# Optimization experiments

Hardware: AMD Instinct MI355X
Metric: run time of the kernel (lower is better)

Reference implementation:

```python
import jax, jax.numpy as jnp
import numpy as np

N, E = 50000, 800000
D_IN, D_HID, D_OUT = 128, 256, 128


def setup_inputs() -> dict:
    key = jax.random.key(0)
    k = jax.random.split(key, 7)
    x = jax.random.normal(k[0], (N, D_IN), dtype=jnp.float32)
    edge_src = jax.random.randint(k[1], (E,), 0, N, dtype=jnp.int32)
    edge_dst = jax.random.randint(k[2], (E,), 0, N, dtype=jnp.int32)
    s1 = 1.0 / np.sqrt(2 * D_IN)
    s2 = 1.0 / np.sqrt(2 * D_HID)
    W1 = jax.random.uniform(k[3], (2 * D_IN, D_HID), jnp.float32, -s1, s1)
    b1 = jax.random.uniform(k[4], (D_HID,), jnp.float32, -s1, s1)
    W2 = jax.random.uniform(k[5], (2 * D_HID, D_OUT), jnp.float32, -s2, s2)
    b2 = jax.random.uniform(k[6], (D_OUT,), jnp.float32, -s2, s2)
    return {"x": x, "edge_src": edge_src, "edge_dst": edge_dst,
            "W1": W1, "b1": b1, "W2": W2, "b2": b2}


def _sage_layer(h, edge_src, edge_dst, W, b, inv_deg):
    # mean-pool neighbor features: gather [E, D] then segment-sum to [N, D]
    msgs = h[edge_src]
    agg = jax.ops.segment_sum(msgs, edge_dst, num_segments=h.shape[0]) * inv_deg
    y = jnp.concatenate([h, agg], axis=1)  # [N, 2D]
    return y @ W + b


def reference(x, edge_src, edge_dst, W1, b1, W2, b2):
    n = x.shape[0]
    deg = jax.ops.segment_sum(jnp.ones_like(edge_dst, dtype=x.dtype), edge_dst,
                              num_segments=n)
    inv_deg = (1.0 / jnp.maximum(deg, 1.0))[:, None]  # isolated nodes -> zeros
    h = _sage_layer(x, edge_src, edge_dst, W1, b1, inv_deg)
    h = jax.nn.relu(h)
    # dropout is identity in eval mode
    h = _sage_layer(h, edge_src, edge_dst, W2, b2, inv_deg)
    return jax.nn.log_softmax(h, axis=1)
```

## Files before the change

kernel.cpp:

```cpp
#include <hip/hip_runtime.h>
#include <cstdint>
#include <cstddef>

typedef __attribute__((ext_vector_type(8))) short bf16x8;
typedef __attribute__((ext_vector_type(4))) float f32x4;
typedef __attribute__((ext_vector_type(2))) float f32x2;

__device__ inline short bf16_rne(float f) {
  unsigned u = __builtin_bit_cast(unsigned, f);
  u += 0x7fff + ((u >> 16) & 1);
  return (short)(u >> 16);
}

__device__ inline float bf16lo(unsigned v) { return __builtin_bit_cast(float, v << 16); }
__device__ inline float bf16hi(unsigned v) { return __builtin_bit_cast(float, v & 0xffff0000u); }

__device__ inline unsigned pack2(float a, float b) {
  return ((unsigned)(unsigned short)bf16_rne(a)) | (((unsigned)(unsigned short)bf16_rne(b)) << 16);
}

__device__ inline void async_copy16(const void* g, void* l) {
  __builtin_amdgcn_global_load_lds((const __attribute__((address_space(1))) void*)g,
                                   (__attribute__((address_space(3))) void*)l, 16, 0, 0);
}


__global__ __launch_bounds__(256) void bucket_hist(const int* __restrict__ dst, int E, int EPB,
                                                   int* __restrict__ histT, int SB, int NB) {
  __shared__ int h[256];
  int tid = threadIdx.x;
  h[tid] = 0;
  __syncthreads();
  int start = blockIdx.x * EPB, end = min(E, start + EPB);
  for (int i = start + tid; i < end; i += 256) atomicAdd(&h[((unsigned)dst[i]) >> 8], 1);
  __syncthreads();
  if (tid < NB) histT[tid * SB + blockIdx.x] = h[tid];
}

__global__ __launch_bounds__(1024) void scan1_kernel(const int* __restrict__ in,
                                                     int* __restrict__ outx,
                                                     int* __restrict__ part, int n) {
  __shared__ int buf[1024];
  int tid = threadIdx.x;
  int i = blockIdx.x * 1024 + tid;
  int v = (i < n) ? in[i] : 0;
  buf[tid] = v;
  __syncthreads();
  #pragma unroll
  for (int off = 1; off < 1024; off <<= 1) {
    int t = (tid >= off) ? buf[tid - off] : 0;
    __syncthreads();
    buf[tid] += t;
    __syncthreads();
  }
  if (i < n) outx[i] = buf[tid] - v;
  if (tid == 1023) part[blockIdx.x] = buf[1023];
}

__global__ __launch_bounds__(1024) void scan2_kernel(int* __restrict__ part, int B) {
  __shared__ int buf[1024];
  int tid = threadIdx.x;
  int v = (tid < B) ? part[tid] : 0;
  buf[tid] = v;
  __syncthreads();
  #pragma unroll
  for (int off = 1; off < 1024; off <<= 1) {
    int t = (tid >= off) ? buf[tid - off] : 0;
    __syncthreads();
    buf[tid] += t;
    __syncthreads();
  }
  if (tid < B) part[tid] = buf[tid] - v;
}

__global__ __launch_bounds__(256) void bucket_scatter(const int* __restrict__ src,
                                                      const int* __restrict__ dst, int E, int EPB,
                                                      const int* __restrict__ excl,
                                                      const int* __restrict__ part, int SB, int NB,
                                                      unsigned* __restrict__ bedge) {
  __shared__ int cur[256];
  int tid = threadIdx.x;
  for (int t = tid; t < NB; t += 256) cur[t] = excl[t * SB + blockIdx.x] + part[t];
  __syncthreads();
  int start = blockIdx.x * EPB, end = min(E, start + EPB);
  for (int i = start + tid; i < end; i += 256) {
    unsigned d = (unsigned)dst[i];
    int p = atomicAdd(&cur[d >> 8], 1);
    bedge[p] = ((d & 255u) << 24) | (unsigned)src[i];
  }
}

__global__ __launch_bounds__(256) void build_csr(const unsigned* __restrict__ bedge,
                                                 const int* __restrict__ excl,
                                                 const int* __restrict__ part, int SB, int NB,
                                                 int N, int E,
                                                 int* __restrict__ offsets,
                                                 float* __restrict__ inv_deg,
                                                 int* __restrict__ ssrc) {
  __shared__ int buf[256];
  int b = blockIdx.x, tid = threadIdx.x;
  int estart = excl[b * SB] + part[b];
  int eend = (b == NB - 1) ? E : (excl[(b + 1) * SB] + part[b + 1]);
  buf[tid] = 0;
  __syncthreads();
  for (int i = estart + tid; i < eend; i += 256) atomicAdd(&buf[bedge[i] >> 24], 1);
  __syncthreads();
  int cnt = buf[tid];
  #pragma unroll
  for (int off = 1; off < 256; off <<= 1) {
    int t = (tid >= off) ? buf[tid - off] : 0;
    __syncthreads();
    buf[tid] += t;
    __syncthreads();
  }
  int excl_l = buf[tid] - cnt;
  int node = (b << 8) + tid;
  if (node < N) {
    offsets[node] = estart + excl_l;
    inv_deg[node] = 1.0f / fmaxf((float)cnt, 1.0f);
  }
  if (node == N) offsets[N] = E;
  __syncthreads();
  buf[tid] = estart + excl_l;
  __syncthreads();
  for (int i = estart + tid; i < eend; i += 256) {
    unsigned e2 = bedge[i];
    int p = atomicAdd(&buf[e2 >> 24], 1);
    ssrc[p] = (int)(e2 & 0xFFFFFFu);
  }
}

__global__ __launch_bounds__(256) void prep_kernel(const float* __restrict__ W1,
                                                   const float* __restrict__ W2,
                                                   const float* __restrict__ b2,
                                                   const float* __restrict__ x,
                                                   short* __restrict__ B1p,
                                                   short* __restrict__ B2p,
                                                   float* __restrict__ bias2,
                                                   unsigned* __restrict__ A1u, int npairs) {
  int b = blockIdx.x;
  if (b < 512) {
    int mode = b >> 8;
    int idx = (b & 255) * 256 + threadIdx.x;
    int j = idx & 7;
    int L = (idx >> 3) & 63;
    int nt = (idx >> 9) & 15;
    int kb = idx >> 13;
    int k = kb * 32 + (L >> 4) * 8 + j;
    int n = nt * 16 + (L & 15);
    if (mode == 0) {
      B1p[idx] = bf16_rne(W1[(size_t)k * 256 + n]);
    } else {
      float v = (n < 128) ? W2[(size_t)k * 128 + n] : W2[(size_t)(256 + k) * 128 + (n - 128)];
      B2p[idx] = bf16_rne(v);
    }
  } else if (b == 512) {
    int j = threadIdx.x;
    bias2[j] = (j < 128) ? b2[j] : 0.0f;
  } else {
    int idx = (b - 513) * 256 + threadIdx.x;
    if (idx < npairs) {
      int n = idx >> 6, dp = idx & 63;
      float2 v = ((const float2*)x)[idx];
      A1u[(size_t)n * 128 + dp] = pack2(v.x, v.y);
    }
  }
}

__global__ __launch_bounds__(256) void agg1_kernel(const uint2* __restrict__ A2,
                                                   const int* __restrict__ offsets,
                                                   const int* __restrict__ ssrc,
                                                   const float* __restrict__ inv_deg,
                                                   uint2* __restrict__ A2out, int N) {
  int node = blockIdx.x * 4 + (threadIdx.x >> 6);
  if (node >= N) return;
  int lane = threadIdx.x & 63;
  int half = lane >> 5;
  int l = lane & 31;
  int s = offsets[node], e = offsets[node + 1];
  float a0 = 0.f, a1 = 0.f, a2 = 0.f, a3 = 0.f;
  int i = s;
  for (; i + 8 <= e; i += 8) {
    int sA = ssrc[i + half], sB = ssrc[i + 2 + half];
    int sC = ssrc[i + 4 + half], sD = ssrc[i + 6 + half];
    uint2 u = A2[((unsigned)sA << 6) + l];
    uint2 v = A2[((unsigned)sB << 6) + l];
    uint2 w = A2[((unsigned)sC << 6) + l];
    uint2 z = A2[((unsigned)sD << 6) + l];
    a0 += bf16lo(u.x); a1 += bf16hi(u.x); a2 += bf16lo(u.y); a3 += bf16hi(u.y);
    a0 += bf16lo(v.x); a1 += bf16hi(v.x); a2 += bf16lo(v.y); a3 += bf16hi(v.y);
    a0 += bf16lo(w.x); a1 += bf16hi(w.x); a2 += bf16lo(w.y); a3 += bf16hi(w.y);
    a0 += bf16lo(z.x); a1 += bf16hi(z.x); a2 += bf16lo(z.y); a3 += bf16hi(z.y);
  }
  for (; i + 2 <= e; i += 2) {
    int sA = ssrc[i + half];
    uint2 u = A2[((unsigned)sA << 6) + l];
    a0 += bf16lo(u.x); a1 += bf16hi(u.x); a2 += bf16lo(u.y); a3 += bf16hi(u.y);
  }
  if (i < e && half == 0) {
    uint2 u = A2[((unsigned)ssrc[i] << 6) + l];
    a0 += bf16lo(u.x); a1 += bf16hi(u.x); a2 += bf16lo(u.y); a3 += bf16hi(u.y);
  }
  a0 += __shfl_xor(a0, 32, 64);
  a1 += __shfl_xor(a1, 32, 64);
  a2 += __shfl_xor(a2, 32, 64);
  a3 += __shfl_xor(a3, 32, 64);
  if (half == 0) {
    float id = inv_deg[node];
    A2out[((unsigned)node << 6) + 32 + l] =
        make_uint2(pack2(a0 * id, a1 * id), pack2(a2 * id, a3 * id));
  }
}

__global__ __launch_bounds__(256) void gemm_mfma(const short* __restrict__ A,
                                                 const short* __restrict__ Bp,
                                                 const float* __restrict__ bias,
                                                 void* __restrict__ out0,
                                                 void* __restrict__ out1,
                                                 int M_pad, int mode) {
  __shared__ __align__(16) short As[4096];
  __shared__ __align__(16) short Bs[4096];
  int tid = threadIdx.x;
  int w = tid >> 6;
  int lane = tid & 63;
  int wr = w >> 1;
  int wc = w & 1;
  int bm = blockIdx.x * 128;
  int bn = blockIdx.y * 128;

  f32x4 acc[4][4];
  #pragma unroll
  for (int i = 0; i < 4; ++i)
    #pragma unroll
    for (int j = 0; j < 4; ++j) acc[i][j] = (f32x4)(0.0f);

  for (int kb = 0; kb < 8; ++kb) {
    #pragma unroll
    for (int q = 0; q < 2; ++q) {
      int f = q * 4 + w;
      int row = bm + f * 16 + (lane & 15);
      const short* g = A + (size_t)row * 256 + kb * 32 + (lane >> 4) * 8;
      async_copy16(g, &As[f * 512]);
    }
    #pragma unroll
    for (int q = 0; q < 2; ++q) {
      int f = q * 4 + w;
      const short* g = Bp + ((size_t)(kb * 16 + (bn >> 4) + f) * 64 + lane) * 8;
      async_copy16(g, &Bs[f * 512]);
    }
    __syncthreads();

    bf16x8 af[4], bfr[4];
    #pragma unroll
    for (int i = 0; i < 4; ++i)
      af[i] = *(const bf16x8*)&As[(wr * 4 + i) * 512 + lane * 8];
    #pragma unroll
    for (int j = 0; j < 4; ++j)
      bfr[j] = *(const bf16x8*)&Bs[(wc * 4 + j) * 512 + lane * 8];

    #pragma unroll
    for (int i = 0; i < 4; ++i)
      #pragma unroll
      for (int j = 0; j < 4; ++j)
        acc[i][j] = __builtin_amdgcn_mfma_f32_16x16x32_bf16(af[i], bfr[j], acc[i][j], 0, 0, 0);
    __syncthreads();
  }

  int crow0 = (lane >> 4) * 4;
  int ccol = lane & 15;
  #pragma unroll
  for (int i = 0; i < 4; ++i) {
    #pragma unroll
    for (int j = 0; j < 4; ++j) {
      int col_loc = wc * 64 + j * 16 + ccol;
      int col = bn + col_loc;
      #pragma unroll
      for (int r = 0; r < 4; ++r) {
        int row = bm + wr * 64 + i * 16 + crow0 + r;
        float v = acc[i][j][r] + bias[col];
        if (mode == 0) {
          v = fmaxf(v, 0.0f);
          ((short*)out0)[(size_t)row * 256 + col] = bf16_rne(v);
        } else if (blockIdx.y == 0) {
          ((short*)out0)[(size_t)row * 128 + col_loc] = bf16_rne(v);
        } else {
          int pk = __builtin_amdgcn_cvt_pk_fp8_f32(v, v, 0, false);
          ((unsigned char*)out1)[(size_t)row * 128 + col_loc] = (unsigned char)(pk & 0xff);
        }
      }
    }
  }
}

__global__ __launch_bounds__(256) void final_kernel(const uint2* __restrict__ utopU,
                                                    const unsigned* __restrict__ T2,
                                                    const int* __restrict__ offsets,
                                                    const int* __restrict__ ssrc,
                                                    const float* __restrict__ inv_deg,
                                                    float4* __restrict__ out4, int N) {
  int node = blockIdx.x * 4 + (threadIdx.x >> 6);
  if (node >= N) return;
  int lane = threadIdx.x & 63;
  int half = lane >> 5;
  int l = lane & 31;
  int s = offsets[node], e = offsets[node + 1];
  float a0 = 0.f, a1 = 0.f, a2 = 0.f, a3 = 0.f;
  int i = s;
  for (; i + 8 <= e; i += 8) {
    int sA = ssrc[i + half], sB = ssrc[i + 2 + half];
    int sC = ssrc[i + 4 + half], sD = ssrc[i + 6 + half];
    unsigned u = T2[((unsigned)sA << 5) + l];
    unsigned v = T2[((unsigned)sB << 5) + l];
    unsigned w = T2[((unsigned)sC << 5) + l];
    unsigned z = T2[((unsigned)sD << 5) + l];
    f32x2 p, q;
    p = __builtin_amdgcn_cvt_pk_f32_fp8(u, false); q = __builtin_amdgcn_cvt_pk_f32_fp8(u, true);
    a0 += p[0]; a1 += p[1]; a2 += q[0]; a3 += q[1];
    p = __builtin_amdgcn_cvt_pk_f32_fp8(v, false); q = __builtin_amdgcn_cvt_pk_f32_fp8(v, true);
    a0 += p[0]; a1 += p[1]; a2 += q[0]; a3 += q[1];
    p = __builtin_amdgcn_cvt_pk_f32_fp8(w, false); q = __builtin_amdgcn_cvt_pk_f32_fp8(w, true);
    a0 += p[0]; a1 += p[1]; a2 += q[0]; a3 += q[1];
    p = __builtin_amdgcn_cvt_pk_f32_fp8(z, false); q = __builtin_amdgcn_cvt_pk_f32_fp8(z, true);
    a0 += p[0]; a1 += p[1]; a2 += q[0]; a3 += q[1];
  }
  for (; i + 2 <= e; i += 2) {
    unsigned u = T2[((unsigned)ssrc[i + half] << 5) + l];
    f32x2 p = __builtin_amdgcn_cvt_pk_f32_fp8(u, false);
    f32x2 q = __builtin_amdgcn_cvt_pk_f32_fp8(u, true);
    a0 += p[0]; a1 += p[1]; a2 += q[0]; a3 += q[1];
  }
  if (i < e && half == 0) {
    unsigned u = T2[((unsigned)ssrc[i] << 5) + l];
    f32x2 p = __builtin_amdgcn_cvt_pk_f32_fp8(u, false);
    f32x2 q = __builtin_amdgcn_cvt_pk_f32_fp8(u, true);
    a0 += p[0]; a1 += p[1]; a2 += q[0]; a3 += q[1];
  }
  a0 += __shfl_xor(a0, 32, 64);
  a1 += __shfl_xor(a1, 32, 64);
  a2 += __shfl_xor(a2, 32, 64);
  a3 += __shfl_xor(a3, 32, 64);
  if (half == 0) {
    float id = inv_deg[node];
    uint2 u = utopU[((unsigned)node << 5) + l];
    float v0 = bf16lo(u.x) + a0 * id;
    float v1 = bf16hi(u.x) + a1 * id;
    float v2 = bf16lo(u.y) + a2 * id;
    float v3 = bf16hi(u.y) + a3 * id;
    float m = fmaxf(fmaxf(v0, v1), fmaxf(v2, v3));
    #pragma unroll
    for (int off = 1; off < 32; off <<= 1) m = fmaxf(m, __shfl_xor(m, off, 32));
    float su = expf(v0 - m) + expf(v1 - m) + expf(v2 - m) + expf(v3 - m);
    #pragma unroll
    for (int off = 1; off < 32; off <<= 1) su += __shfl_xor(su, off, 32);
    float ls = m + logf(su);
    out4[((unsigned)node << 5) + l] = make_float4(v0 - ls, v1 - ls, v2 - ls, v3 - ls);
  }
}

extern "C" void kernel_launch(void* const* d_in, const int* in_sizes, int n_in,
                              void* d_out, int out_size, void* d_ws, size_t ws_size,
                              hipStream_t stream) {
  const float* x        = (const float*)d_in[0];
  const int*   edge_src = (const int*)d_in[1];
  const int*   edge_dst = (const int*)d_in[2];
  const float* W1       = (const float*)d_in[3];
  const float* b1       = (const float*)d_in[4];
  const float* W2       = (const float*)d_in[5];
  const float* b2       = (const float*)d_in[6];
  float* out = (float*)d_out;

  const int D_IN = 128;
  const int N = in_sizes[0] / D_IN;
  const int E = in_sizes[1];
  const int M_pad = ((N + 127) / 128) * 128;

  const int SB = 1024;
  const int EPB = (E + SB - 1) / SB;
  const int NB = (N + 255) >> 8;
  const int M = NB * SB;
  const int sbl = (M + 1023) / 1024;

  char* ws = (char*)d_ws;
  size_t p = 0;
  auto take = [&](size_t bytes) -> size_t {
    size_t r = p;
    p += (bytes + 255) & ~(size_t)255;
    return r;
  };
  size_t histT_off = take((size_t)M * 4);
  size_t excl_off  = take((size_t)(M + 1) * 4);
  size_t part_off  = take((size_t)1024 * 4);
  size_t bedge_off = take((size_t)E * 4);
  size_t offs_off  = take((size_t)(N + 1) * 4);
  size_t inv_off   = take((size_t)N * 4);
  size_t ssrc_off  = take((size_t)E * 4);
  size_t A1_off    = take((size_t)M_pad * 256 * 2);
  size_t h_off     = take((size_t)M_pad * 256 * 2);
  size_t B1p_off   = take((size_t)256 * 256 * 2);
  size_t B2p_off   = take((size_t)256 * 256 * 2);
  size_t bias2_off = take((size_t)256 * 4);
  size_t utop_off  = take((size_t)M_pad * 128 * 2);
  size_t t2_off    = take((size_t)M_pad * 128);
  (void)ws_size;

  int*   histT   = (int*)(ws + histT_off);
  int*   excl    = (int*)(ws + excl_off);
  int*   part    = (int*)(ws + part_off);
  unsigned* bedge = (unsigned*)(ws + bedge_off);
  int*   offsets = (int*)(ws + offs_off);
  float* inv_deg = (float*)(ws + inv_off);
  int*   ssrc    = (int*)(ws + ssrc_off);
  unsigned* A1u  = (unsigned*)(ws + A1_off);
  short* h       = (short*)(ws + h_off);
  short* B1p     = (short*)(ws + B1p_off);
  short* B2p     = (short*)(ws + B2p_off);
  float* bias2   = (float*)(ws + bias2_off);
  short* utop    = (short*)(ws + utop_off);
  unsigned char* t2f8 = (unsigned char*)(ws + t2_off);

  bucket_hist<<<SB, 256, 0, stream>>>(edge_dst, E, EPB, histT, SB, NB);
  scan1_kernel<<<sbl, 1024, 0, stream>>>(histT, excl, part, M);
  scan2_kernel<<<1, 1024, 0, stream>>>(part, sbl);
  bucket_scatter<<<SB, 256, 0, stream>>>(edge_src, edge_dst, E, EPB, excl, part, SB, NB, bedge);
  build_csr<<<NB, 256, 0, stream>>>(bedge, excl, part, SB, NB, N, E, offsets, inv_deg, ssrc);

  {
    int npairs = N * 64;
    int grid = 513 + (npairs + 255) / 256;
    prep_kernel<<<grid, 256, 0, stream>>>(W1, W2, b2, x, B1p, B2p, bias2, A1u, npairs);
  }

  agg1_kernel<<<(N + 3) / 4, 256, 0, stream>>>((const uint2*)A1u, offsets, ssrc, inv_deg,
                                               (uint2*)A1u, N);
  {
    dim3 grid(M_pad / 128, 2);
    gemm_mfma<<<grid, 256, 0, stream>>>((const short*)A1u, B1p, b1, h, nullptr, M_pad, 0);
  }
  {
    dim3 grid(M_pad / 128, 2);
    gemm_mfma<<<grid, 256, 0, stream>>>(h, B2p, bias2, utop, t2f8, M_pad, 1);
  }
  final_kernel<<<(N + 3) / 4, 256, 0, stream>>>((const uint2*)utop, (const unsigned*)t2f8,
                                                offsets, ssrc, inv_deg, (float4*)out, N);
}
```

Baseline: 240.2 us.

## Gather layer-1 neighbors from FP8 copy of x and widen per-lane gather width

The prep kernel now also writes an FP8 (e4m3) copy of the input features, and the first aggregation gathers neighbor rows from it instead of the bf16 copy, halving gather bytes per edge. Both gather kernels change to four edge-groups of 16 lanes, each loading 8 bytes and accumulating 8 channels, with a two-step shuffle reduction. The CSR bucket size drops from 256 to 128 nodes, giving more build_csr blocks. FP8 quantization of the raw inputs adds error to the layer-1 mean aggregation.

```diff
diff --git a/kernel.cpp b/kernel.cpp
--- a/kernel.cpp
+++ b/kernel.cpp
@@ -27,14 +27,14 @@
 
 __global__ __launch_bounds__(256) void bucket_hist(const int* __restrict__ dst, int E, int EPB,
                                                    int* __restrict__ histT, int SB, int NB) {
-  __shared__ int h[256];
+  __shared__ int h[512];
   int tid = threadIdx.x;
-  h[tid] = 0;
+  for (int t = tid; t < NB; t += 256) h[t] = 0;
   __syncthreads();
   int start = blockIdx.x * EPB, end = min(E, start + EPB);
-  for (int i = start + tid; i < end; i += 256) atomicAdd(&h[((unsigned)dst[i]) >> 8], 1);
-  __syncthreads();
-  if (tid < NB) histT[tid * SB + blockIdx.x] = h[tid];
+  for (int i = start + tid; i < end; i += 256) atomicAdd(&h[((unsigned)dst[i]) >> 7], 1);
+  __syncthreads();
+  for (int t = tid; t < NB; t += 256) histT[t * SB + blockIdx.x] = h[t];
 }
 
 __global__ __launch_bounds__(1024) void scan1_kernel(const int* __restrict__ in,
@@ -78,15 +78,15 @@
                                                       const int* __restrict__ excl,
                                                       const int* __restrict__ part, int SB, int NB,
                                                       unsigned* __restrict__ bedge) {
-  __shared__ int cur[256];
+  __shared__ int cur[512];
   int tid = threadIdx.x;
   for (int t = tid; t < NB; t += 256) cur[t] = excl[t * SB + blockIdx.x] + part[t];
   __syncthreads();
   int start = blockIdx.x * EPB, end = min(E, start + EPB);
   for (int i = start + tid; i < end; i += 256) {
     unsigned d = (unsigned)dst[i];
-    int p = atomicAdd(&cur[d >> 8], 1);
-    bedge[p] = ((d & 255u) << 24) | (unsigned)src[i];
+    int p = atomicAdd(&cur[d >> 7], 1);
+    bedge[p] = ((d & 127u) << 24) | (unsigned)src[i];
   }
 }
 
@@ -97,31 +97,32 @@
                                                  int* __restrict__ offsets,
                                                  float* __restrict__ inv_deg,
                                                  int* __restrict__ ssrc) {
-  __shared__ int buf[256];
+  __shared__ int buf[128];
   int b = blockIdx.x, tid = threadIdx.x;
   int estart = excl[b * SB] + part[b];
   int eend = (b == NB - 1) ? E : (excl[(b + 1) * SB] + part[b + 1]);
-  buf[tid] = 0;
+  if (tid < 128) buf[tid] = 0;
   __syncthreads();
   for (int i = estart + tid; i < eend; i += 256) atomicAdd(&buf[bedge[i] >> 24], 1);
   __syncthreads();
-  int cnt = buf[tid];
+  int cnt = (tid < 128) ? buf[tid] : 0;
   #pragma unroll
-  for (int off = 1; off < 256; off <<= 1) {
-    int t = (tid >= off) ? buf[tid - off] : 0;
-    __syncthreads();
-    buf[tid] += t;
-    __syncthreads();
-  }
-  int excl_l = buf[tid] - cnt;
-  int node = (b << 8) + tid;
-  if (node < N) {
-    offsets[node] = estart + excl_l;
-    inv_deg[node] = 1.0f / fmaxf((float)cnt, 1.0f);
-  }
-  if (node == N) offsets[N] = E;
-  __syncthreads();
-  buf[tid] = estart + excl_l;
+  for (int off = 1; off < 128; off <<= 1) {
+    int t = (tid >= off && tid < 128) ? buf[tid - off] : 0;
+    __syncthreads();
+    if (tid < 128) buf[tid] += t;
+    __syncthreads();
+  }
+  if (tid < 128) {
+    int excl_l = buf[tid] - cnt;
+    int node = (b << 7) + tid;
+    if (node < N) {
+      offsets[node] = estart + excl_l;
+      inv_deg[node] = 1.0f / fmaxf((float)cnt, 1.0f);
+    }
+    if (node == N) offsets[N] = E;
+    buf[tid] = estart + excl_l;
+  }
   __syncthreads();
   for (int i = estart + tid; i < eend; i += 256) {
     unsigned e2 = bedge[i];
@@ -137,7 +138,8 @@
                                                    short* __restrict__ B1p,
                                                    short* __restrict__ B2p,
                                                    float* __restrict__ bias2,
-                                                   unsigned* __restrict__ A1u, int npairs) {
+                                                   unsigned* __restrict__ A1u,
+                                                   unsigned* __restrict__ xf8, int nquads) {
   int b = blockIdx.x;
   if (b < 512) {
     int mode = b >> 8;
@@ -159,56 +161,68 @@
     bias2[j] = (j < 128) ? b2[j] : 0.0f;
   } else {
     int idx = (b - 513) * 256 + threadIdx.x;
-    if (idx < npairs) {
-      int n = idx >> 6, dp = idx & 63;
-      float2 v = ((const float2*)x)[idx];
-      A1u[(size_t)n * 128 + dp] = pack2(v.x, v.y);
-    }
-  }
-}
-
-__global__ __launch_bounds__(256) void agg1_kernel(const uint2* __restrict__ A2,
+    if (idx < nquads) {
+      int n = idx >> 5, q = idx & 31;
+      float4 v = ((const float4*)x)[idx];
+      ((uint2*)A1u)[(size_t)n * 64 + q] = make_uint2(pack2(v.x, v.y), pack2(v.z, v.w));
+      int pk = __builtin_amdgcn_cvt_pk_fp8_f32(v.x, v.y, 0, false);
+      pk = __builtin_amdgcn_cvt_pk_fp8_f32(v.z, v.w, pk, true);
+      xf8[(size_t)n * 32 + q] = (unsigned)pk;
+    }
+  }
+}
+
+
+__global__ __launch_bounds__(256) void agg1_kernel(const uint2* __restrict__ X8,
                                                    const int* __restrict__ offsets,
                                                    const int* __restrict__ ssrc,
                                                    const float* __restrict__ inv_deg,
-                                                   uint2* __restrict__ A2out, int N) {
+                                                   uint4* __restrict__ A1q, int N) {
   int node = blockIdx.x * 4 + (threadIdx.x >> 6);
   if (node >= N) return;
   int lane = threadIdx.x & 63;
-  int half = lane >> 5;
-  int l = lane & 31;
+  int g = lane >> 4;
+  int l = lane & 15;
   int s = offsets[node], e = offsets[node + 1];
-  float a0 = 0.f, a1 = 0.f, a2 = 0.f, a3 = 0.f;
+  float a0=0.f,a1=0.f,a2=0.f,a3=0.f,a4=0.f,a5=0.f,a6=0.f,a7=0.f;
   int i = s;
   for (; i + 8 <= e; i += 8) {
-    int sA = ssrc[i + half], sB = ssrc[i + 2 + half];
-    int sC = ssrc[i + 4 + half], sD = ssrc[i + 6 + half];
-    uint2 u = A2[((unsigned)sA << 6) + l];
-    uint2 v = A2[((unsigned)sB << 6) + l];
-    uint2 w = A2[((unsigned)sC << 6) + l];
-    uint2 z = A2[((unsigned)sD << 6) + l];
-    a0 += bf16lo(u.x); a1 += bf16hi(u.x); a2 += bf16lo(u.y); a3 += bf16hi(u.y);
-    a0 += bf16lo(v.x); a1 += bf16hi(v.x); a2 += bf16lo(v.y); a3 += bf16hi(v.y);
-    a0 += bf16lo(w.x); a1 += bf16hi(w.x); a2 += bf16lo(w.y); a3 += bf16hi(w.y);
-    a0 += bf16lo(z.x); a1 += bf16hi(z.x); a2 += bf16lo(z.y); a3 += bf16hi(z.y);
-  }
-  for (; i + 2 <= e; i += 2) {
-    int sA = ssrc[i + half];
-    uint2 u = A2[((unsigned)sA << 6) + l];
-    a0 += bf16lo(u.x); a1 += bf16hi(u.x); a2 += bf16lo(u.y); a3 += bf16hi(u.y);
-  }
-  if (i < e && half == 0) {
-    uint2 u = A2[((unsigned)ssrc[i] << 6) + l];
-    a0 += bf16lo(u.x); a1 += bf16hi(u.x); a2 += bf16lo(u.y); a3 += bf16hi(u.y);
-  }
-  a0 += __shfl_xor(a0, 32, 64);
-  a1 += __shfl_xor(a1, 32, 64);
-  a2 += __shfl_xor(a2, 32, 64);
-  a3 += __shfl_xor(a3, 32, 64);
-  if (half == 0) {
+    int sA = ssrc[i + g], sB = ssrc[i + 4 + g];
+    uint2 u = X8[((size_t)(unsigned)sA << 4) + l];
+    uint2 v = X8[((size_t)(unsigned)sB << 4) + l];
+    f32x2 p, q;
+    p = __builtin_amdgcn_cvt_pk_f32_fp8(u.x, false); q = __builtin_amdgcn_cvt_pk_f32_fp8(u.x, true);
+    a0 += p[0]; a1 += p[1]; a2 += q[0]; a3 += q[1];
+    p = __builtin_amdgcn_cvt_pk_f32_fp8(u.y, false); q = __builtin_amdgcn_cvt_pk_f32_fp8(u.y, true);
+    a4 += p[0]; a5 += p[1]; a6 += q[0]; a7 += q[1];
+    p = __builtin_amdgcn_cvt_pk_f32_fp8(v.x, false); q = __builtin_amdgcn_cvt_pk_f32_fp8(v.x, true);
+    a0 += p[0]; a1 += p[1]; a2 += q[0]; a3 += q[1];
+    p = __builtin_amdgcn_cvt_pk_f32_fp8(v.y, false); q = __builtin_amdgcn_cvt_pk_f32_fp8(v.y, true);
+    a4 += p[0]; a5 += p[1]; a6 += q[0]; a7 += q[1];
+  }
+  for (; i < e; i += 4) {
+    if (g < e - i) {
+      uint2 u = X8[((size_t)(unsigned)ssrc[i + g] << 4) + l];
+      f32x2 p, q;
+      p = __builtin_amdgcn_cvt_pk_f32_fp8(u.x, false); q = __builtin_amdgcn_cvt_pk_f32_fp8(u.x, true);
+      a0 += p[0]; a1 += p[1]; a2 += q[0]; a3 += q[1];
+      p = __builtin_amdgcn_cvt_pk_f32_fp8(u.y, false); q = __builtin_amdgcn_cvt_pk_f32_fp8(u.y, true);
+      a4 += p[0]; a5 += p[1]; a6 += q[0]; a7 += q[1];
+    }
+  }
+  a0 += __shfl_xor(a0,16,64); a0 += __shfl_xor(a0,32,64);
+  a1 += __shfl_xor(a1,16,64); a1 += __shfl_xor(a1,32,64);
+  a2 += __shfl_xor(a2,16,64); a2 += __shfl_xor(a2,32,64);
+  a3 += __shfl_xor(a3,16,64); a3 += __shfl_xor(a3,32,64);
+  a4 += __shfl_xor(a4,16,64); a4 += __shfl_xor(a4,32,64);
+  a5 += __shfl_xor(a5,16,64); a5 += __shfl_xor(a5,32,64);
+  a6 += __shfl_xor(a6,16,64); a6 += __shfl_xor(a6,32,64);
+  a7 += __shfl_xor(a7,16,64); a7 += __shfl_xor(a7,32,64);
+  if (g == 0) {
     float id = inv_deg[node];
-    A2out[((unsigned)node << 6) + 32 + l] =
-        make_uint2(pack2(a0 * id, a1 * id), pack2(a2 * id, a3 * id));
+    A1q[((size_t)node << 5) + 16 + l] =
+        make_uint4(pack2(a0 * id, a1 * id), pack2(a2 * id, a3 * id),
+                   pack2(a4 * id, a5 * id), pack2(a6 * id, a7 * id));
   }
 }
 
@@ -292,8 +306,8 @@
   }
 }
 
-__global__ __launch_bounds__(256) void final_kernel(const uint2* __restrict__ utopU,
-                                                    const unsigned* __restrict__ T2,
+__global__ __launch_bounds__(256) void final_kernel(const uint4* __restrict__ utopq,
+                                                    const uint2* __restrict__ T2,
                                                     const int* __restrict__ offsets,
                                                     const int* __restrict__ ssrc,
                                                     const float* __restrict__ inv_deg,
@@ -301,59 +315,64 @@
   int node = blockIdx.x * 4 + (threadIdx.x >> 6);
   if (node >= N) return;
   int lane = threadIdx.x & 63;
-  int half = lane >> 5;
-  int l = lane & 31;
+  int g = lane >> 4;
+  int l = lane & 15;
   int s = offsets[node], e = offsets[node + 1];
-  float a0 = 0.f, a1 = 0.f, a2 = 0.f, a3 = 0.f;
+  float a0=0.f,a1=0.f,a2=0.f,a3=0.f,a4=0.f,a5=0.f,a6=0.f,a7=0.f;
   int i = s;
   for (; i + 8 <= e; i += 8) {
-    int sA = ssrc[i + half], sB = ssrc[i + 2 + half];
-    int sC = ssrc[i + 4 + half], sD = ssrc[i + 6 + half];
-    unsigned u = T2[((unsigned)sA << 5) + l];
-    unsigned v = T2[((unsigned)sB << 5) + l];
-    unsigned w = T2[((unsigned)sC << 5) + l];
-    unsigned z = T2[((unsigned)sD << 5) + l];
+    int sA = ssrc[i + g], sB = ssrc[i + 4 + g];
+    uint2 u = T2[((size_t)(unsigned)sA << 4) + l];
+    uint2 v = T2[((size_t)(unsigned)sB << 4) + l];
     f32x2 p, q;
-    p = __builtin_amdgcn_cvt_pk_f32_fp8(u, false); q = __builtin_amdgcn_cvt_pk_f32_fp8(u, true);
+    p = __builtin_amdgcn_cvt_pk_f32_fp8(u.x, false); q = __builtin_amdgcn_cvt_pk_f32_fp8(u.x, true);
     a0 += p[0]; a1 += p[1]; a2 += q[0]; a3 += q[1];
-    p = __builtin_amdgcn_cvt_pk_f32_fp8(v, false); q = __builtin_amdgcn_cvt_pk_f32_fp8(v, true);
+    p = __builtin_amdgcn_cvt_pk_f32_fp8(u.y, false); q = __builtin_amdgcn_cvt_pk_f32_fp8(u.y, true);
+    a4 += p[0]; a5 += p[1]; a6 += q[0]; a7 += q[1];
+    p = __builtin_amdgcn_cvt_pk_f32_fp8(v.x, false); q = __builtin_amdgcn_cvt_pk_f32_fp8(v.x, true);
     a0 += p[0]; a1 += p[1]; a2 += q[0]; a3 += q[1];
-    p = __builtin_amdgcn_cvt_pk_f32_fp8(w, false); q = __builtin_amdgcn_cvt_pk_f32_fp8(w, true);
-    a0 += p[0]; a1 += p[1]; a2 += q[0]; a3 += q[1];
-    p = __builtin_amdgcn_cvt_pk_f32_fp8(z, false); q = __builtin_amdgcn_cvt_pk_f32_fp8(z, true);
-    a0 += p[0]; a1 += p[1]; a2 += q[0]; a3 += q[1];
-  }
-  for (; i + 2 <= e; i += 2) {
-    unsigned u = T2[((unsigned)ssrc[i + half] << 5) + l];
-    f32x2 p = __builtin_amdgcn_cvt_pk_f32_fp8(u, false);
-    f32x2 q = __builtin_amdgcn_cvt_pk_f32_fp8(u, true);
-    a0 += p[0]; a1 += p[1]; a2 += q[0]; a3 += q[1];
-  }
-  if (i < e && half == 0) {
-    unsigned u = T2[((unsigned)ssrc[i] << 5) + l];
-    f32x2 p = __builtin_amdgcn_cvt_pk_f32_fp8(u, false);
-    f32x2 q = __builtin_amdgcn_cvt_pk_f32_fp8(u, true);
-    a0 += p[0]; a1 += p[1]; a2 += q[0]; a3 += q[1];
-  }
-  a0 += __shfl_xor(a0, 32, 64);
-  a1 += __shfl_xor(a1, 32, 64);
-  a2 += __shfl_xor(a2, 32, 64);
-  a3 += __shfl_xor(a3, 32, 64);
-  if (half == 0) {
+    p = __builtin_amdgcn_cvt_pk_f32_fp8(v.y, false); q = __builtin_amdgcn_cvt_pk_f32_fp8(v.y, true);
+    a4 += p[0]; a5 += p[1]; a6 += q[0]; a7 += q[1];
+  }
+  for (; i < e; i += 4) {
+    if (g < e - i) {
+      uint2 u = T2[((size_t)(unsigned)ssrc[i + g] << 4) + l];
+      f32x2 p, q;
+      p = __builtin_amdgcn_cvt_pk_f32_fp8(u.x, false); q = __builtin_amdgcn_cvt_pk_f32_fp8(u.x, true);
+      a0 += p[0]; a1 += p[1]; a2 += q[0]; a3 += q[1];
+      p = __builtin_amdgcn_cvt_pk_f32_fp8(u.y, false); q = __builtin_amdgcn_cvt_pk_f32_fp8(u.y, true);
+      a4 += p[0]; a5 += p[1]; a6 += q[0]; a7 += q[1];
+    }
+  }
+  a0 += __shfl_xor(a0,16,64); a0 += __shfl_xor(a0,32,64);
+  a1 += __shfl_xor(a1,16,64); a1 += __shfl_xor(a1,32,64);
+  a2 += __shfl_xor(a2,16,64); a2 += __shfl_xor(a2,32,64);
+  a3 += __shfl_xor(a3,16,64); a3 += __shfl_xor(a3,32,64);
+  a4 += __shfl_xor(a4,16,64); a4 += __shfl_xor(a4,32,64);
+  a5 += __shfl_xor(a5,16,64); a5 += __shfl_xor(a5,32,64);
+  a6 += __shfl_xor(a6,16,64); a6 += __shfl_xor(a6,32,64);
+  a7 += __shfl_xor(a7,16,64); a7 += __shfl_xor(a7,32,64);
+  if (g == 0) {
     float id = inv_deg[node];
-    uint2 u = utopU[((unsigned)node << 5) + l];
-    float v0 = bf16lo(u.x) + a0 * id;
-    float v1 = bf16hi(u.x) + a1 * id;
-    float v2 = bf16lo(u.y) + a2 * id;
-    float v3 = bf16hi(u.y) + a3 * id;
-    float m = fmaxf(fmaxf(v0, v1), fmaxf(v2, v3));
-    #pragma unroll
-    for (int off = 1; off < 32; off <<= 1) m = fmaxf(m, __shfl_xor(m, off, 32));
-    float su = expf(v0 - m) + expf(v1 - m) + expf(v2 - m) + expf(v3 - m);
-    #pragma unroll
-    for (int off = 1; off < 32; off <<= 1) su += __shfl_xor(su, off, 32);
+    uint4 U = utopq[((size_t)node << 4) + l];
+    float v0 = bf16lo(U.x) + a0 * id;
+    float v1 = bf16hi(U.x) + a1 * id;
+    float v2 = bf16lo(U.y) + a2 * id;
+    float v3 = bf16hi(U.y) + a3 * id;
+    float v4 = bf16lo(U.z) + a4 * id;
+    float v5 = bf16hi(U.z) + a5 * id;
+    float v6 = bf16lo(U.w) + a6 * id;
+    float v7 = bf16hi(U.w) + a7 * id;
+    float m = fmaxf(fmaxf(fmaxf(v0, v1), fmaxf(v2, v3)), fmaxf(fmaxf(v4, v5), fmaxf(v6, v7)));
+    #pragma unroll
+    for (int off = 1; off < 16; off <<= 1) m = fmaxf(m, __shfl_xor(m, off, 16));
+    float su = expf(v0 - m) + expf(v1 - m) + expf(v2 - m) + expf(v3 - m) +
+               expf(v4 - m) + expf(v5 - m) + expf(v6 - m) + expf(v7 - m);
+    #pragma unroll
+    for (int off = 1; off < 16; off <<= 1) su += __shfl_xor(su, off, 16);
     float ls = m + logf(su);
-    out4[((unsigned)node << 5) + l] = make_float4(v0 - ls, v1 - ls, v2 - ls, v3 - ls);
+    out4[((size_t)node << 5) + l * 2]     = make_float4(v0 - ls, v1 - ls, v2 - ls, v3 - ls);
+    out4[((size_t)node << 5) + l * 2 + 1] = make_float4(v4 - ls, v5 - ls, v6 - ls, v7 - ls);
   }
 }
 
@@ -376,7 +395,7 @@
 
   const int SB = 1024;
   const int EPB = (E + SB - 1) / SB;
-  const int NB = (N + 255) >> 8;
+  const int NB = (N + 127) >> 7;
   const int M = NB * SB;
   const int sbl = (M + 1023) / 1024;
 
@@ -395,6 +414,7 @@
   size_t inv_off   = take((size_t)N * 4);
   size_t ssrc_off  = take((size_t)E * 4);
   size_t A1_off    = take((size_t)M_pad * 256 * 2);
+  size_t xf8_off   = take((size_t)M_pad * 128);
   size_t h_off     = take((size_t)M_pad * 256 * 2);
   size_t B1p_off   = take((size_t)256 * 256 * 2);
   size_t B2p_off   = take((size_t)256 * 256 * 2);
@@ -411,6 +431,7 @@
   float* inv_deg = (float*)(ws + inv_off);
   int*   ssrc    = (int*)(ws + ssrc_off);
   unsigned* A1u  = (unsigned*)(ws + A1_off);
+  unsigned* xf8  = (unsigned*)(ws + xf8_off);
   short* h       = (short*)(ws + h_off);
   short* B1p     = (short*)(ws + B1p_off);
   short* B2p     = (short*)(ws + B2p_off);
@@ -425,13 +446,13 @@
   build_csr<<<NB, 256, 0, stream>>>(bedge, excl, part, SB, NB, N, E, offsets, inv_deg, ssrc);
 
   {
-    int npairs = N * 64;
-    int grid = 513 + (npairs + 255) / 256;
-    prep_kernel<<<grid, 256, 0, stream>>>(W1, W2, b2, x, B1p, B2p, bias2, A1u, npairs);
-  }
-
-  agg1_kernel<<<(N + 3) / 4, 256, 0, stream>>>((const uint2*)A1u, offsets, ssrc, inv_deg,
-                                               (uint2*)A1u, N);
+    int nquads = N * 32;
+    int grid = 513 + (nquads + 255) / 256;
+    prep_kernel<<<grid, 256, 0, stream>>>(W1, W2, b2, x, B1p, B2p, bias2, A1u, xf8, nquads);
+  }
+
+  agg1_kernel<<<(N + 3) / 4, 256, 0, stream>>>((const uint2*)xf8, offsets, ssrc, inv_deg,
+                                               (uint4*)A1u, N);
   {
     dim3 grid(M_pad / 128, 2);
     gemm_mfma<<<grid, 256, 0, stream>>>((const short*)A1u, B1p, b1, h, nullptr, M_pad, 0);
@@ -440,6 +461,6 @@
     dim3 grid(M_pad / 128, 2);
     gemm_mfma<<<grid, 256, 0, stream>>>(h, B2p, bias2, utop, t2f8, M_pad, 1);
   }
-  final_kernel<<<(N + 3) / 4, 256, 0, stream>>>((const uint2*)utop, (const unsigned*)t2f8,
+  final_kernel<<<(N + 3) / 4, 256, 0, stream>>>((const uint4*)utop, (const uint2*)t2f8,
                                                 offsets, ssrc, inv_deg, (float4*)out, N);
 }
```

New measurement: 236.9 us. No clear change (-1.4%).
